# Performance work log

Hardware: AMD Instinct MI355X
Metric: run time of the kernel (lower is better)

Reference implementation:

```python
import jax, jax.numpy as jnp
import numpy as np


def _mlp(h, W_in, b_in, W_hid, b_hid, W_out, b_out):
    # 392 -> 1000 -> (1000)x4 -> 392, ReLU between linear layers (NICE shift net)
    h = jax.nn.relu(h @ W_in + b_in)
    for i in range(W_hid.shape[0]):  # fixed small layer count, not a data dim
        h = jax.nn.relu(h @ W_hid[i] + b_hid[i])
    return h @ W_out + b_out


def setup_inputs() -> dict:
    key = jax.random.key(0)
    ks = jax.random.split(key, 4)
    B, D, MID = 4096, 784, 1000
    half = D // 2
    return {
        "x": jax.random.normal(ks[0], (B, D), jnp.float32),
        "log_det_J": jnp.zeros((1,), jnp.float32),
        "W_in": jax.random.normal(ks[1], (half, MID), jnp.float32) * 0.05,
        "b_in": jnp.zeros((MID,), jnp.float32),
        "W_hid": jax.random.normal(ks[2], (4, MID, MID), jnp.float32) * 0.03,
        "b_hid": jnp.zeros((4, MID), jnp.float32),
        "W_out": jax.random.normal(ks[3], (MID, half), jnp.float32) * 0.03,
        "b_out": jnp.zeros((half,), jnp.float32),
    }


def reference(x, log_det_J, W_in, b_in, W_hid, b_hid, W_out, b_out):
    # mask_config = 0: first = even columns, second = odd columns
    first = x[:, 0::2]   # (B, D/2)
    second = x[:, 1::2]  # (B, D/2)
    shift = _mlp(first, W_in, b_in, W_hid, b_hid, W_out, b_out)
    y_second = second + shift  # coupling_law (reverse=False)
    # interleave: y[:, 0::2] = first, y[:, 1::2] = y_second, in one strided write
    y = jnp.stack([first, y_second], axis=2).reshape(x.shape)
    return (y, log_det_J)
```

## Files before the change

### kernel.cpp

```cpp
#include <hip/hip_runtime.h>

typedef __bf16 bf16;
typedef __bf16 bf16x8 __attribute__((ext_vector_type(8)));
typedef float f32x4 __attribute__((ext_vector_type(4)));

#define M_TOT 4096
#define D_IN  784
#define HALF  392
#define MID   1000
#define K0PAD 448
#define NPAD  1024

__device__ __forceinline__ void g2l16(const bf16* g, bf16* l) {
  __builtin_amdgcn_global_load_lds(
      (__attribute__((address_space(1))) void*)(g),
      (__attribute__((address_space(3))) void*)(l),
      16, 0, 0);
}

__device__ __forceinline__ void wtrans_tile(const float* __restrict__ W, bf16* __restrict__ WT,
                                            int K, int N, int Kpad, int tn, int tk,
                                            float (*tb)[33], int tid) {
  int n0 = tn * 32, k0 = tk * 32;
  int tx = tid & 31, ty = tid >> 5;
#pragma unroll
  for (int r = 0; r < 4; ++r) {
    int k = k0 + ty + 8 * r, n = n0 + tx;
    tb[ty + 8 * r][tx] = (k < K && n < N) ? W[(size_t)k * N + n] : 0.f;
  }
  __syncthreads();
#pragma unroll
  for (int r = 0; r < 4; ++r) {
    int n = n0 + ty + 8 * r, k = k0 + tx;
    WT[(size_t)n * Kpad + k] = (bf16)tb[tx][ty + 8 * r];
  }
}

__global__ void prep_k(const float* __restrict__ x, const float* __restrict__ ldj,
                       const float* __restrict__ W_in, const float* __restrict__ W_hid,
                       const float* __restrict__ W_out,
                       bf16* __restrict__ A0, bf16* __restrict__ WT0,
                       bf16* __restrict__ WTh, bf16* __restrict__ WT5,
                       float* __restrict__ y) {
  __shared__ float tb[32][33];
  const int b = blockIdx.x, tid = threadIdx.x;
  if (b < 896) {
    int g = b * 256 + tid;
    int m = g / 56;
    int kq = g - m * 56, k0 = kq * 8;
    bf16x8 v;
    if (k0 < HALF) {
      const float4* xr = (const float4*)(x + (size_t)m * D_IN + 2 * k0);
      float4 a0 = xr[0], a1 = xr[1], a2 = xr[2], a3 = xr[3];
      v[0] = (bf16)a0.x; v[1] = (bf16)a0.z;
      v[2] = (bf16)a1.x; v[3] = (bf16)a1.z;
      v[4] = (bf16)a2.x; v[5] = (bf16)a2.z;
      v[6] = (bf16)a3.x; v[7] = (bf16)a3.z;
    } else {
#pragma unroll
      for (int j = 0; j < 8; ++j) v[j] = (bf16)0.f;
    }
    *(bf16x8*)(A0 + (size_t)m * K0PAD + k0) = v;
    if (b == 0 && tid == 0) y[(size_t)M_TOT * D_IN] = ldj[0];
    return;
  }
  int t = b - 896;
  const float* W; bf16* WT; int K, N, Kpad, tn, tk;
  if (t < 448) {
    W = W_in; WT = WT0; K = HALF; N = MID; Kpad = K0PAD;
    tn = t & 31; tk = t >> 5;
  } else if (t < 4544) {
    int u = t - 448; int i = u >> 10; u &= 1023;
    W = W_hid + (size_t)i * MID * MID; WT = WTh + (size_t)i * NPAD * NPAD;
    K = MID; N = MID; Kpad = NPAD;
    tn = u & 31; tk = u >> 5;
  } else {
    int u = t - 4544;
    W = W_out; WT = WT5; K = MID; N = HALF; Kpad = NPAD;
    tn = u & 15; tk = u >> 4;
  }
  wtrans_tile(W, WT, K, N, Kpad, tn, tk, tb, tid);
}

template <int EPI, int K>
__global__ __launch_bounds__(256)
void gemm_k(const bf16* __restrict__ A, const bf16* __restrict__ BT,
            const float* __restrict__ bias, int bias_n,
            bf16* __restrict__ C,
            const float* __restrict__ x, float* __restrict__ y) {
  constexpr int BM = 128, BN = 128, BK = 64, NBUF = 4;
  constexpr int MT = BM / 32, NT = BN / 32;
  constexpr int KT = K / BK;
  constexpr int NBM = M_TOT / BM;
  constexpr int AI = (BM / 4) / 8;
  constexpr int BI = (BN / 4) / 8;
  constexpr int LPS = AI + BI;
  static_assert(K % BK == 0 && KT >= NBUF, "K/BK");
  static_assert(LPS == 8, "vmcnt immediates assume LPS=8");

  alignas(16) __shared__ bf16 ldsA[NBUF][BM * BK];
  alignas(16) __shared__ bf16 ldsB[NBUF][BN * BK];
  const int tid = threadIdx.x;
  const int id = blockIdx.x;

  const int wave = tid >> 6, lane = tid & 63;
  const int bm = id % NBM, bn = id / NBM;

  const int srow = lane >> 3;
  const int scol = lane & 7;
  const bf16* gAb = A + ((size_t)bm * BM + wave * (BM / 4)) * K;
  const bf16* gBb = BT + ((size_t)bn * BN + wave * (BN / 4)) * K;
  const int lAo = wave * (BM / 4) * BK;
  const int lBo = wave * (BN / 4) * BK;

  const int mlane = lane & 15, quad = lane >> 4;
  const int wm = (wave & 1) * (BM / 2), wn = (wave >> 1) * (BN / 2);
  const int axor = mlane & 7;

  auto stage = [&](int kt, int pb) {
    const int koff = kt * BK;
#pragma unroll
    for (int i = 0; i < AI; ++i) {
      int r = i * 8 + srow;
      g2l16(gAb + (size_t)r * K + koff + (scol ^ (r & 7)) * 8,
            &ldsA[pb][lAo + i * 8 * BK]);
    }
#pragma unroll
    for (int i = 0; i < BI; ++i) {
      int r = i * 8 + srow;
      g2l16(gBb + (size_t)r * K + koff + (scol ^ (r & 7)) * 8,
            &ldsB[pb][lBo + i * 8 * BK]);
    }
  };

  f32x4 acc[MT][NT] = {};

  stage(0, 0); stage(1, 1); stage(2, 2); stage(3, 3);

  for (int kt = 0; kt < KT; ++kt) {
    const int pb = kt & 3;
    const int rem = KT - 1 - kt;
    if (rem >= 3)
      asm volatile("s_waitcnt vmcnt(24)" ::: "memory");
    else if (rem == 2)
      asm volatile("s_waitcnt vmcnt(16)" ::: "memory");
    else if (rem == 1)
      asm volatile("s_waitcnt vmcnt(8)" ::: "memory");
    else
      asm volatile("s_waitcnt vmcnt(0)" ::: "memory");
    __builtin_amdgcn_s_barrier();
    __builtin_amdgcn_sched_barrier(0);

    const bf16* raB = &ldsA[pb][(wm + mlane) * BK];
    const bf16* rbB = &ldsB[pb][(wn + mlane) * BK];
    bf16x8 af[2][MT], bfr[2][NT];
#pragma unroll
    for (int s = 0; s < 2; ++s) {
      const int co = ((s * 4 + quad) ^ axor) * 8;
#pragma unroll
      for (int i = 0; i < MT; ++i) af[s][i] = *(const bf16x8*)(raB + i * 16 * BK + co);
#pragma unroll
      for (int i = 0; i < NT; ++i) bfr[s][i] = *(const bf16x8*)(rbB + i * 16 * BK + co);
    }
    asm volatile("s_waitcnt lgkmcnt(0)" ::: "memory");
    __builtin_amdgcn_sched_barrier(0);
    __builtin_amdgcn_s_barrier();
    __builtin_amdgcn_sched_barrier(0);

    if (kt + NBUF < KT) stage(kt + NBUF, pb);

#pragma unroll
    for (int s = 0; s < 2; ++s)
#pragma unroll
      for (int mt = 0; mt < MT; ++mt)
#pragma unroll
        for (int nt = 0; nt < NT; ++nt)
          acc[mt][nt] = __builtin_amdgcn_mfma_f32_16x16x32_bf16(
              af[s][mt], bfr[s][nt], acc[mt][nt], 0, 0, 0);
  }

  const int ng0 = bn * BN + wn + mlane;
  const int mg0 = bm * BM + wm + quad * 4;

  if (EPI == 0) {
    float bv[NT];
#pragma unroll
    for (int nt = 0; nt < NT; ++nt) {
      int n = ng0 + nt * 16;
      bv[nt] = (n < bias_n) ? bias[n] : 0.f;
    }
#pragma unroll
    for (int mt = 0; mt < MT; ++mt)
#pragma unroll
      for (int nt = 0; nt < NT; ++nt)
#pragma unroll
        for (int r = 0; r < 4; ++r) {
          int m = mg0 + mt * 16 + r;
          int n = ng0 + nt * 16;
          float v = fmaxf(acc[mt][nt][r] + bv[nt], 0.f);
          C[(size_t)m * NPAD + n] = (bf16)v;
        }
  } else {
    const float2* x2 = (const float2*)x;
    float2* y2 = (float2*)y;
#pragma unroll
    for (int nt = 0; nt < NT; ++nt) {
      int n = ng0 + nt * 16;
      if (n < HALF) {
        float bb = bias[n];
#pragma unroll
        for (int mt = 0; mt < MT; ++mt)
#pragma unroll
          for (int r = 0; r < 4; ++r) {
            int m = mg0 + mt * 16 + r;
            size_t off = (size_t)m * (D_IN / 2) + n;
            float2 v = x2[off];
            v.y += acc[mt][nt][r] + bb;
            y2[off] = v;
          }
      }
    }
  }
}

extern "C" void kernel_launch(void* const* d_in, const int* in_sizes, int n_in,
                              void* d_out, int out_size, void* d_ws, size_t ws_size,
                              hipStream_t stream) {
  const float* x     = (const float*)d_in[0];
  const float* ldj   = (const float*)d_in[1];
  const float* W_in  = (const float*)d_in[2];
  const float* b_in  = (const float*)d_in[3];
  const float* W_hid = (const float*)d_in[4];
  const float* b_hid = (const float*)d_in[5];
  const float* W_out = (const float*)d_in[6];
  const float* b_out = (const float*)d_in[7];
  float* y = (float*)d_out;

  char* p = (char*)d_ws;
  bf16* A0  = (bf16*)(p + 0);
  bf16* H0  = (bf16*)(p + 3670016);
  bf16* H1  = (bf16*)(p + 12058624);
  bf16* WT0 = (bf16*)(p + 20447232);
  bf16* WTh = (bf16*)(p + 21364736);
  bf16* WT5 = (bf16*)(p + 29753344);

  const size_t WH = (size_t)NPAD * NPAD;

  prep_k<<<dim3(896 + 5056), 256, 0, stream>>>(x, ldj, W_in, W_hid, W_out,
                                               A0, WT0, WTh, WT5, y);

  gemm_k<0, K0PAD><<<dim3(256), 256, 0, stream>>>(A0, WT0, b_in, MID, H0, nullptr, nullptr);
  gemm_k<0, NPAD><<<dim3(256), 256, 0, stream>>>(H0, WTh + 0 * WH, b_hid + 0 * MID, MID, H1, nullptr, nullptr);
  gemm_k<0, NPAD><<<dim3(256), 256, 0, stream>>>(H1, WTh + 1 * WH, b_hid + 1 * MID, MID, H0, nullptr, nullptr);
  gemm_k<0, NPAD><<<dim3(256), 256, 0, stream>>>(H0, WTh + 2 * WH, b_hid + 2 * MID, MID, H1, nullptr, nullptr);
  gemm_k<0, NPAD><<<dim3(256), 256, 0, stream>>>(H1, WTh + 3 * WH, b_hid + 3 * MID, MID, H0, nullptr, nullptr);
  gemm_k<1, NPAD><<<dim3(128), 256, 0, stream>>>(H0, WT5, b_out, HALF, nullptr, x, y);
}
```

Baseline: 187.1 us.

## Use three-stage LDS pipeline, compute before refill, narrower tiles for output GEMM

Result: slower. 196.8 us (+5.2%).

```diff
diff --git a/kernel.cpp b/kernel.cpp
--- a/kernel.cpp
+++ b/kernel.cpp
@@ -82,13 +82,13 @@
   wtrans_tile(W, WT, K, N, Kpad, tn, tk, tb, tid);
 }
 
-template <int EPI, int K>
+template <int BM, int BN, int EPI, int K>
 __global__ __launch_bounds__(256)
 void gemm_k(const bf16* __restrict__ A, const bf16* __restrict__ BT,
             const float* __restrict__ bias, int bias_n,
             bf16* __restrict__ C,
             const float* __restrict__ x, float* __restrict__ y) {
-  constexpr int BM = 128, BN = 128, BK = 64, NBUF = 4;
+  constexpr int BK = 64, NBUF = 3;
   constexpr int MT = BM / 32, NT = BN / 32;
   constexpr int KT = K / BK;
   constexpr int NBM = M_TOT / BM;
@@ -96,7 +96,6 @@
   constexpr int BI = (BN / 4) / 8;
   constexpr int LPS = AI + BI;
   static_assert(K % BK == 0 && KT >= NBUF, "K/BK");
-  static_assert(LPS == 8, "vmcnt immediates assume LPS=8");
 
   alignas(16) __shared__ bf16 ldsA[NBUF][BM * BK];
   alignas(16) __shared__ bf16 ldsB[NBUF][BN * BK];
@@ -135,17 +134,15 @@
 
   f32x4 acc[MT][NT] = {};
 
-  stage(0, 0); stage(1, 1); stage(2, 2); stage(3, 3);
-
+  stage(0, 0); stage(1, 1); stage(2, 2);
+
+  int pb = 0;
   for (int kt = 0; kt < KT; ++kt) {
-    const int pb = kt & 3;
     const int rem = KT - 1 - kt;
-    if (rem >= 3)
-      asm volatile("s_waitcnt vmcnt(24)" ::: "memory");
-    else if (rem == 2)
-      asm volatile("s_waitcnt vmcnt(16)" ::: "memory");
+    if (rem >= 2)
+      asm volatile("s_waitcnt vmcnt(%0)" ::"n"(2 * LPS) : "memory");
     else if (rem == 1)
-      asm volatile("s_waitcnt vmcnt(8)" ::: "memory");
+      asm volatile("s_waitcnt vmcnt(%0)" ::"n"(LPS) : "memory");
     else
       asm volatile("s_waitcnt vmcnt(0)" ::: "memory");
     __builtin_amdgcn_s_barrier();
@@ -162,21 +159,22 @@
 #pragma unroll
       for (int i = 0; i < NT; ++i) bfr[s][i] = *(const bf16x8*)(rbB + i * 16 * BK + co);
     }
+#pragma unroll
+    for (int s = 0; s < 2; ++s)
+#pragma unroll
+      for (int mt = 0; mt < MT; ++mt)
+#pragma unroll
+        for (int nt = 0; nt < NT; ++nt)
+          acc[mt][nt] = __builtin_amdgcn_mfma_f32_16x16x32_bf16(
+              af[s][mt], bfr[s][nt], acc[mt][nt], 0, 0, 0);
+
     asm volatile("s_waitcnt lgkmcnt(0)" ::: "memory");
     __builtin_amdgcn_sched_barrier(0);
     __builtin_amdgcn_s_barrier();
     __builtin_amdgcn_sched_barrier(0);
 
     if (kt + NBUF < KT) stage(kt + NBUF, pb);
-
-#pragma unroll
-    for (int s = 0; s < 2; ++s)
-#pragma unroll
-      for (int mt = 0; mt < MT; ++mt)
-#pragma unroll
-        for (int nt = 0; nt < NT; ++nt)
-          acc[mt][nt] = __builtin_amdgcn_mfma_f32_16x16x32_bf16(
-              af[s][mt], bfr[s][nt], acc[mt][nt], 0, 0, 0);
+    pb = (pb + 1 == NBUF) ? 0 : pb + 1;
   }
 
   const int ng0 = bn * BN + wn + mlane;
@@ -249,10 +247,16 @@
   prep_k<<<dim3(896 + 5056), 256, 0, stream>>>(x, ldj, W_in, W_hid, W_out,
                                                A0, WT0, WTh, WT5, y);
 
-  gemm_k<0, K0PAD><<<dim3(256), 256, 0, stream>>>(A0, WT0, b_in, MID, H0, nullptr, nullptr);
-  gemm_k<0, NPAD><<<dim3(256), 256, 0, stream>>>(H0, WTh + 0 * WH, b_hid + 0 * MID, MID, H1, nullptr, nullptr);
-  gemm_k<0, NPAD><<<dim3(256), 256, 0, stream>>>(H1, WTh + 1 * WH, b_hid + 1 * MID, MID, H0, nullptr, nullptr);
-  gemm_k<0, NPAD><<<dim3(256), 256, 0, stream>>>(H0, WTh + 2 * WH, b_hid + 2 * MID, MID, H1, nullptr, nullptr);
-  gemm_k<0, NPAD><<<dim3(256), 256, 0, stream>>>(H1, WTh + 3 * WH, b_hid + 3 * MID, MID, H0, nullptr, nullptr);
-  gemm_k<1, NPAD><<<dim3(128), 256, 0, stream>>>(H0, WT5, b_out, HALF, nullptr, x, y);
-}
+  gemm_k<128, 128, 0, K0PAD><<<dim3(256), 256, 0, stream>>>(
+      A0, WT0, b_in, MID, H0, nullptr, nullptr);
+  gemm_k<128, 128, 0, NPAD><<<dim3(256), 256, 0, stream>>>(
+      H0, WTh + 0 * WH, b_hid + 0 * MID, MID, H1, nullptr, nullptr);
+  gemm_k<128, 128, 0, NPAD><<<dim3(256), 256, 0, stream>>>(
+      H1, WTh + 1 * WH, b_hid + 1 * MID, MID, H0, nullptr, nullptr);
+  gemm_k<128, 128, 0, NPAD><<<dim3(256), 256, 0, stream>>>(
+      H0, WTh + 2 * WH, b_hid + 2 * MID, MID, H1, nullptr, nullptr);
+  gemm_k<128, 128, 0, NPAD><<<dim3(256), 256, 0, stream>>>(
+      H1, WTh + 3 * WH, b_hid + 3 * MID, MID, H0, nullptr, nullptr);
+  gemm_k<128, 64, 1, NPAD><<<dim3(256), 256, 0, stream>>>(
+      H0, WT5, b_out, HALF, nullptr, x, y);
+}
```
